# Kernel tuning notes

Measured on AMD Instinct MI355X. Metric: run time of the kernel, lower is better.

The kernel has to match this reference:

```python
import jax, jax.numpy as jnp
import numpy as np

N_NODES = 100000
N_EDGES = 3200000
IN_DIM, HID, OUT_DIM = 1, 64, 1


def graph_conv(x, src, dst, ew, W_rel, b_rel, W_root):
    # PyG GraphConv (aggr='add'): out_i = W_rel @ sum_{j->i} w_ij x_j + b_rel + W_root @ x_i
    msg = x[src] * ew[:, None]                               # [E, F]
    agg = jax.ops.segment_sum(msg, dst, num_segments=N_NODES)  # [N, F]
    return agg @ W_rel + b_rel + x @ W_root


def setup_inputs() -> dict:
    key = jax.random.key(0)
    ks = jax.random.split(key, 12)
    def glorot(k, shape):
        fan_in, fan_out = shape
        lim = float(np.sqrt(6.0 / (fan_in + fan_out)))
        return jax.random.uniform(k, shape, jnp.float32, -lim, lim)
    x = jax.random.normal(ks[0], (N_NODES, IN_DIM), jnp.float32)
    edge_index = jax.random.randint(ks[1], (2, N_EDGES), 0, N_NODES, jnp.int64)
    edge_weight = jax.random.uniform(ks[2], (N_EDGES,), jnp.float32)
    return {
        "x": x, "edge_index": edge_index, "edge_weight": edge_weight,
        "W1_rel": glorot(ks[3], (IN_DIM, HID)), "b1": jnp.zeros((HID,), jnp.float32),
        "W1_root": glorot(ks[4], (IN_DIM, HID)),
        "W2_rel": glorot(ks[5], (HID, HID)), "b2": jnp.zeros((HID,), jnp.float32),
        "W2_root": glorot(ks[6], (HID, HID)),
        "W3_rel": glorot(ks[7], (HID, OUT_DIM)), "b3": jnp.zeros((OUT_DIM,), jnp.float32),
        "W3_root": glorot(ks[8], (HID, OUT_DIM)),
    }


def reference(x, edge_index, edge_weight, W1_rel, b1, W1_root, W2_rel, b2, W2_root, W3_rel, b3, W3_root):
    src, dst = edge_index[0], edge_index[1]
    h = graph_conv(x, src, dst, edge_weight, W1_rel, b1, W1_root)
    h = jax.nn.relu(h)  # dropout is identity in eval mode
    h = graph_conv(h, src, dst, edge_weight, W2_rel, b2, W2_root)
    h = jax.nn.relu(h)
    return graph_conv(h, src, dst, edge_weight, W3_rel, b3, W3_root)
```

## Files before the change

kernel.cpp:

```cpp
#include <hip/hip_runtime.h>

#define NN 100000
#define NE 3200000
#define HID 64
#define NPB 256
#define NB  ((NN + NPB - 1) / NPB)
#define NNP (NB * NPB)
#define CAP 9216
#define MNP 128
#define NMW (2 * NB)
#define CAPW 5120
#define CHUNK 4096
#define NCH ((NE + CHUNK - 1) / CHUNK)
#define AP 72
#define BPITCH 136
#define SRCM 0x1FFFF

typedef _Float16 half8 __attribute__((ext_vector_type(8)));
typedef _Float16 h2v   __attribute__((ext_vector_type(2)));
typedef float f32x4 __attribute__((ext_vector_type(4)));

__device__ __forceinline__ unsigned short f2hb(float v) {
    _Float16 h = (_Float16)v;
    unsigned short s;
    __builtin_memcpy(&s, &h, 2);
    return s;
}
__device__ __forceinline__ h2v ash2(unsigned int u) {
    h2v r;
    __builtin_memcpy(&r, &u, 4);
    return r;
}

__global__ __launch_bounds__(512) void k_init(int* __restrict__ gcur) {
    if (threadIdx.x < NB) gcur[threadIdx.x] = threadIdx.x * CAP;
}

__global__ __launch_bounds__(256) void k_scatter(const int* __restrict__ src,
                                                 const int* __restrict__ dst,
                                                 const float* __restrict__ ew,
                                                 int* __restrict__ gcur,
                                                 int2* __restrict__ rec,
                                                 unsigned char* __restrict__ dlb) {
    __shared__ int2 lrec[CHUNK];
    __shared__ unsigned short lb[CHUNK];
    __shared__ unsigned short sidx[CHUNK];
    __shared__ int cnt[NB];
    __shared__ int bme[NB];
    __shared__ int wt8[8];
    const int tid = threadIdx.x;
    const int lane = tid & 63, wvx = tid >> 6;
    for (int j = tid; j < NB; j += 256) cnt[j] = 0;
    __syncthreads();
    const long long b0 = (long long)blockIdx.x * CHUNK;
    const int valid = (int)min((long long)CHUNK, (long long)NE - b0);
    #pragma unroll
    for (int k = 0; k < CHUNK / 256; ++k) {
        int idx = k * 256 + tid;
        if (idx < valid) {
            long long e = b0 + idx;
            int d = dst[e];
            int b = d >> 8;
            lrec[idx] = make_int2(src[e] | ((d & 255) << 17), __float_as_int(ew[e]));
            lb[idx] = (unsigned short)b;
            atomicAdd(&cnt[b], 1);
        }
    }
    __syncthreads();
    int v0 = (tid < NB) ? cnt[tid] : 0;
    int v1 = (tid + 256 < NB) ? cnt[tid + 256] : 0;
    int i0 = v0, i1 = v1;
    #pragma unroll
    for (int off = 1; off < 64; off <<= 1) {
        int t0 = __shfl_up(i0, off, 64);
        int t1 = __shfl_up(i1, off, 64);
        if (lane >= off) { i0 += t0; i1 += t1; }
    }
    if (lane == 63) { wt8[wvx] = i0; wt8[4 + wvx] = i1; }
    __syncthreads();
    int off0 = 0, off1 = 0;
    #pragma unroll
    for (int j = 0; j < 8; ++j) {
        int wt = wt8[j];
        if (j < wvx) off0 += wt;
        if (j < 4 + wvx) off1 += wt;
    }
    const int excl0 = off0 + i0 - v0;
    const int excl1 = off1 + i1 - v1;
    if (tid < NB) {
        int bb = v0 ? atomicAdd(&gcur[tid], v0) : 0;
        bme[tid] = bb - excl0;
        cnt[tid] = excl0;
    }
    if (tid + 256 < NB) {
        int bb = v1 ? atomicAdd(&gcur[tid + 256], v1) : 0;
        bme[tid + 256] = bb - excl1;
        cnt[tid + 256] = excl1;
    }
    __syncthreads();
    #pragma unroll
    for (int k = 0; k < CHUNK / 256; ++k) {
        int idx = k * 256 + tid;
        if (idx < valid) {
            int sp = atomicAdd(&cnt[lb[idx]], 1);
            sidx[sp] = (unsigned short)idx;
        }
    }
    __syncthreads();
    #pragma unroll
    for (int k = 0; k < CHUNK / 256; ++k) {
        int sp = k * 256 + tid;
        if (sp < valid) {
            int idx = sidx[sp];
            int b = lb[idx];
            int2 rc = lrec[idx];
            int go = bme[b] + sp;
            rec[go] = rc;
            dlb[go] = (unsigned char)((rc.x >> 17) & 255);
        }
    }
}

__global__ __launch_bounds__(512) void k_s1(const int* __restrict__ gcur,
                                            const int2* __restrict__ rec,
                                            const float* __restrict__ x,
                                            float2* __restrict__ sx) {
    __shared__ float loc[NPB];
    if (threadIdx.x < NPB) loc[threadIdx.x] = 0.f;
    __syncthreads();
    const int b = blockIdx.x;
    const int beg = b * CAP, cnt = gcur[b] - beg;
    for (int t = threadIdx.x; t < cnt; t += 512) {
        int2 rc = rec[beg + t];
        atomicAdd(&loc[rc.x >> 17], __int_as_float(rc.y) * x[rc.x & SRCM]);
    }
    __syncthreads();
    int i = b * NPB + threadIdx.x;
    if (threadIdx.x < NPB && i < NN) sx[i] = make_float2(loc[threadIdx.x], x[i]);
}

__global__ __launch_bounds__(512) void k_pack(const int* __restrict__ gcur,
                                              const int2* __restrict__ rec,
                                              const unsigned char* __restrict__ dlb,
                                              const float2* __restrict__ sx,
                                              int4* __restrict__ rec2q,
                                              int* __restrict__ noff,
                                              unsigned char* __restrict__ ngrp) {
    __shared__ int4 img4[CAPW / 2];
    __shared__ int hist[128];
    __shared__ int exclp[128];
    __shared__ int cur[128];
    __shared__ int wt2[2];
    unsigned short* imgh = (unsigned short*)img4;
    const int tid = threadIdx.x;
    const int lane = tid & 63, wv = tid >> 6;
    const int wid = blockIdx.x;
    const int b = wid >> 1, h = wid & 1;
    for (int j = tid; j < CAPW / 2; j += 512) img4[j] = (int4){0, 0, 0, 0};
    if (tid < 128) hist[tid] = 0;
    __syncthreads();
    const int beg = b * CAP;
    const int cnt = gcur[b] - beg;
    {
        const uchar4* d4 = (const uchar4*)(dlb + beg);
        const int n4 = cnt >> 2;
        for (int t = tid; t < n4; t += 512) {
            uchar4 q = d4[t];
            if ((q.x >> 7) == h) atomicAdd(&hist[q.x & 127], 1);
            if ((q.y >> 7) == h) atomicAdd(&hist[q.y & 127], 1);
            if ((q.z >> 7) == h) atomicAdd(&hist[q.z & 127], 1);
            if ((q.w >> 7) == h) atomicAdd(&hist[q.w & 127], 1);
        }
        for (int t = (n4 << 2) + tid; t < cnt; t += 512) {
            int dl = dlb[beg + t];
            if ((dl >> 7) == h) atomicAdd(&hist[dl & 127], 1);
        }
    }
    __syncthreads();
    int pc = 0, incl = 0;
    if (tid < 128) { pc = (hist[tid] + 7) & ~7; incl = pc; }
    #pragma unroll
    for (int off = 1; off < 64; off <<= 1) {
        int tt = __shfl_up(incl, off, 64);
        if (lane >= off) incl += tt;
    }
    if (tid < 128 && lane == 63) wt2[wv] = incl;
    __syncthreads();
    if (tid < 128) {
        int e0 = ((tid >= 64) ? wt2[0] : 0) + incl - pc;
        exclp[tid] = e0;
        cur[tid] = e0;
        const int node = wid * MNP + tid;
        noff[node] = wid * CAPW + e0;
        ngrp[node] = (unsigned char)(pc >> 3);
    }
    __syncthreads();
#define PREC(RX, RY) {                                                  \
        const int dl_ = ((RX) >> 17) & 255;                             \
        if ((dl_ >> 7) == h) {                                          \
            const float w_ = __int_as_float(RY);                        \
            const float2 v_ = sx[(RX) & SRCM];                          \
            int gs_ = atomicAdd(&cur[dl_ & 127], 1);                    \
            int hb_ = (gs_ >> 1) * 8 + (gs_ & 1);                       \
            imgh[hb_]     = f2hb(w_ * v_.x);                            \
            imgh[hb_ + 2] = f2hb(w_ * v_.y);                            \
            imgh[hb_ + 4] = f2hb(w_);                                   \
        } }
    {
        const int4* r4 = (const int4*)(rec + beg);
        const int n2 = cnt >> 1;
        for (int t = tid; t < n2; t += 512) {
            int4 q = r4[t];
            PREC(q.x, q.y)
            PREC(q.z, q.w)
        }
        for (int t = (n2 << 1) + tid; t < cnt; t += 512) {
            int2 rc = rec[beg + t];
            PREC(rc.x, rc.y)
        }
    }
#undef PREC
    __syncthreads();
    int4* d4 = rec2q + (size_t)wid * (CAPW / 2);
    for (int j = tid; j < CAPW / 2; j += 512) d4[j] = img4[j];
}

__global__ __launch_bounds__(512) void k_mega(
        const int* __restrict__ noff, const unsigned char* __restrict__ ngrp,
        const char* __restrict__ rec2b, const float2* __restrict__ sx,
        const float* __restrict__ W1_rel, const float* __restrict__ W1_root,
        const float* __restrict__ b1,
        const float* __restrict__ W2_rel, const float* __restrict__ b2,
        const float* __restrict__ W2_root,
        const float* __restrict__ W3_rel, const float* __restrict__ W3_root,
        float* __restrict__ p, float* __restrict__ r) {
    __shared__ _Float16 aggh[MNP * AP];
    __shared__ _Float16 Bt[HID * BPITCH];
    __shared__ float2 sxl[MNP];
    const int tid = threadIdx.x;
    const int f = tid & 63;
    const int wv = tid >> 6;
    const int gi0 = blockIdx.x * MNP;

    for (int j = tid; j < MNP * AP / 2; j += 512) ((int*)aggh)[j] = 0;
    for (int idx = tid; idx < HID * HID; idx += 512) {
        int k = idx >> 6, n = idx & 63;
        Bt[n * BPITCH + k]       = (_Float16)W2_rel[idx];
        Bt[n * BPITCH + HID + k] = (_Float16)W2_root[idx];
    }
    if (tid < MNP) {
        int gi = gi0 + tid;
        sxl[tid] = (gi < NN) ? sx[gi] : make_float2(0.f, 0.f);
    }
    const float w1rf = W1_rel[f], w1tf = W1_root[f], b1ff = b1[f];
    __syncthreads();

    {
        const int first = gi0 + wv * 16;
        int soff = __builtin_amdgcn_readfirstlane(noff[first]);
        const int4 gvv = *(const int4*)(ngrp + first);
        unsigned ua = __builtin_amdgcn_readfirstlane((unsigned)gvv.x);
        unsigned ub = __builtin_amdgcn_readfirstlane((unsigned)gvv.y);
        unsigned uc = __builtin_amdgcn_readfirstlane((unsigned)gvv.z);
        unsigned ud = __builtin_amdgcn_readfirstlane((unsigned)gvv.w);
        unsigned long long clo = (unsigned long long)ua | ((unsigned long long)ub << 32);
        unsigned long long chi = (unsigned long long)uc | ((unsigned long long)ud << 32);
        #define BSUM(u) (((u) & 255u) + (((u) >> 8) & 255u) + (((u) >> 16) & 255u) + ((u) >> 24))
        const int tg = (int)(BSUM(ua) + BSUM(ub) + BSUM(uc) + BSUM(ud));
        #undef BSUM

        const h2v w1r2 = {(_Float16)w1rf, (_Float16)w1rf};
        const h2v w1t2 = {(_Float16)w1tf, (_Float16)w1tf};
        const h2v b1f2 = {(_Float16)b1ff, (_Float16)b1ff};
        const h2v one2 = {(_Float16)1.f, (_Float16)1.f};
        const h2v zero2 = {(_Float16)0.f, (_Float16)0.f};

        float a0 = 0.f, a1 = 0.f, a2 = 0.f, a3 = 0.f;
        int nrow = wv * 16;
        const int rowend = nrow + 16;
        int grem = (int)(clo & 255); clo = (clo >> 8) | (chi << 56); chi >>= 8;
        while (grem == 0 && nrow + 1 < rowend) {
            ++nrow; grem = (int)(clo & 255);
            clo = (clo >> 8) | (chi << 56); chi >>= 8;
        }

        const int4* rp = (const int4*)rec2b + (soff >> 1);
        int4 A0, A1, A2, A3, B0, B1, B2, B3, C0, C1, C2, C3, D0, D1, D2, D3;
        if (tg >= 1) { A0 = rp[0]; A1 = rp[1]; A2 = rp[2];  A3 = rp[3]; }
        if (tg >= 2) { B0 = rp[4]; B1 = rp[5]; B2 = rp[6];  B3 = rp[7]; }
        if (tg >= 3) { C0 = rp[8]; C1 = rp[9]; C2 = rp[10]; C3 = rp[11]; }
        rp += 12;

#define PP(Q, AA) {                                          \
        h2v z_ = ash2((unsigned)(Q).z) * b1f2;               \
        z_ = ash2((unsigned)(Q).y) * w1t2 + z_;              \
        z_ = ash2((unsigned)(Q).x) * w1r2 + z_;              \
        z_ = __builtin_elementwise_max(z_, zero2);           \
        AA = __builtin_amdgcn_fdot2(z_, one2, AA, false); }

#define BNDRY() {                                                        \
        if (--grem == 0) {                                               \
            aggh[nrow * AP + f] = (_Float16)((a0 + a1) + (a2 + a3));     \
            a0 = a1 = a2 = a3 = 0.f;                                     \
            ++nrow; grem = (int)(clo & 255);                             \
            clo = (clo >> 8) | (chi << 56); chi >>= 8;                   \
            while (grem == 0 && nrow + 1 < rowend) {                     \
                ++nrow; grem = (int)(clo & 255);                         \
                clo = (clo >> 8) | (chi << 56); chi >>= 8;               \
            }                                                            \
        } }

        int t = 0;
        while (t + 4 <= tg) {
            D0 = rp[0]; D1 = rp[1]; D2 = rp[2]; D3 = rp[3];
            PP(A0, a0) PP(A1, a1) PP(A2, a2) PP(A3, a3) BNDRY(); ++t;
            A0 = rp[4]; A1 = rp[5]; A2 = rp[6]; A3 = rp[7];
            PP(B0, a0) PP(B1, a1) PP(B2, a2) PP(B3, a3) BNDRY(); ++t;
            B0 = rp[8]; B1 = rp[9]; B2 = rp[10]; B3 = rp[11];
            PP(C0, a0) PP(C1, a1) PP(C2, a2) PP(C3, a3) BNDRY(); ++t;
            C0 = rp[12]; C1 = rp[13]; C2 = rp[14]; C3 = rp[15];
            PP(D0, a0) PP(D1, a1) PP(D2, a2) PP(D3, a3) BNDRY(); ++t;
            rp += 16;
        }
        if (t < tg) {
            PP(A0, a0) PP(A1, a1) PP(A2, a2) PP(A3, a3) BNDRY(); ++t;
            if (t < tg) {
                PP(B0, a0) PP(B1, a1) PP(B2, a2) PP(B3, a3) BNDRY(); ++t;
                if (t < tg) {
                    PP(C0, a0) PP(C1, a1) PP(C2, a2) PP(C3, a3) BNDRY(); ++t;
                }
            }
        }
#undef PP
#undef BNDRY
    }
    __syncthreads();

    const int m16 = tid & 15;
    const int quad = (tid & 63) >> 4;
    f32x4 acc[4];
    #pragma unroll
    for (int c_ = 0; c_ < 4; ++c_) acc[c_] = (f32x4){0.f, 0.f, 0.f, 0.f};

    const float2 sm = sxl[wv * 16 + m16];

    #pragma unroll
    for (int kt = 0; kt < 4; ++kt) {
        const int kk = kt * 32;
        half8 af;
        if (kt < 2) {
            af = *(const half8*)&aggh[(wv * 16 + m16) * AP + kk + quad * 8];
        } else {
            const int fk0 = (kt - 2) * 32 + quad * 8;
            #pragma unroll
            for (int j = 0; j < 8; ++j) {
                const float wr = W1_rel[fk0 + j], wt = W1_root[fk0 + j], bb = b1[fk0 + j];
                af[j] = (_Float16)fmaxf(0.f, fmaf(sm.x, wr, fmaf(sm.y, wt, bb)));
            }
        }
        #pragma unroll
        for (int ct = 0; ct < 4; ++ct) {
            const half8 bfrag = *(const half8*)&Bt[(ct * 16 + m16) * BPITCH + kk + quad * 8];
            acc[ct] = __builtin_amdgcn_mfma_f32_16x16x32_f16(af, bfrag, acc[ct], 0, 0, 0);
        }
    }

    float b2c[4], w3rc[4], w3tc[4];
    #pragma unroll
    for (int ct = 0; ct < 4; ++ct) {
        const int col = ct * 16 + m16;
        b2c[ct] = b2[col]; w3rc[ct] = W3_rel[col]; w3tc[ct] = W3_root[col];
    }
    float pv[4] = {0.f, 0.f, 0.f, 0.f}, rv[4] = {0.f, 0.f, 0.f, 0.f};
    #pragma unroll
    for (int ct = 0; ct < 4; ++ct) {
        #pragma unroll
        for (int reg = 0; reg < 4; ++reg) {
            const float h2_ = fmaxf(0.f, acc[ct][reg] + b2c[ct]);
            pv[reg] = fmaf(h2_, w3rc[ct], pv[reg]);
            rv[reg] = fmaf(h2_, w3tc[ct], rv[reg]);
        }
    }
    #pragma unroll
    for (int reg = 0; reg < 4; ++reg) {
        #pragma unroll
        for (int msk = 1; msk < 16; msk <<= 1) {
            pv[reg] += __shfl_xor(pv[reg], msk, 64);
            rv[reg] += __shfl_xor(rv[reg], msk, 64);
        }
    }
    if (m16 == 0) {
        #pragma unroll
        for (int reg = 0; reg < 4; ++reg) {
            const int gi = gi0 + wv * 16 + quad * 4 + reg;
            if (gi < NN) { p[gi] = pv[reg]; r[gi] = rv[reg]; }
        }
    }
}

__global__ __launch_bounds__(512) void k_out(const int* __restrict__ gcur,
                                             const int2* __restrict__ rec,
                                             const float* __restrict__ pp,
                                             const float* __restrict__ rr,
                                             const float* __restrict__ b3,
                                             float* __restrict__ out) {
    __shared__ float loc[NPB];
    if (threadIdx.x < NPB) loc[threadIdx.x] = 0.f;
    __syncthreads();
    const int b = blockIdx.x;
    const int beg = b * CAP, cnt = gcur[b] - beg;
    for (int t = threadIdx.x; t < cnt; t += 512) {
        int2 rc = rec[beg + t];
        atomicAdd(&loc[rc.x >> 17], __int_as_float(rc.y) * pp[rc.x & SRCM]);
    }
    __syncthreads();
    int i = b * NPB + threadIdx.x;
    if (threadIdx.x < NPB && i < NN) out[i] = loc[threadIdx.x] + rr[i] + b3[0];
}

extern "C" void kernel_launch(void* const* d_in, const int* in_sizes, int n_in,
                              void* d_out, int out_size, void* d_ws, size_t ws_size,
                              hipStream_t stream) {
    const float* x       = (const float*)d_in[0];
    const int*   ei      = (const int*)  d_in[1];
    const float* ew      = (const float*)d_in[2];
    const float* W1_rel  = (const float*)d_in[3];
    const float* b1      = (const float*)d_in[4];
    const float* W1_root = (const float*)d_in[5];
    const float* W2_rel  = (const float*)d_in[6];
    const float* b2      = (const float*)d_in[7];
    const float* W2_root = (const float*)d_in[8];
    const float* W3_rel  = (const float*)d_in[9];
    const float* b3      = (const float*)d_in[10];
    const float* W3_root = (const float*)d_in[11];

    const int* src = ei;
    const int* dst = ei + NE;

    const size_t REC_SLOTS = (size_t)NB * CAP;
    int2*          rec   = (int2*)d_ws;
    float2*        sx    = (float2*)(rec + REC_SLOTS);
    float*         p     = (float*)(sx + NN);
    float*         r     = p + NN;
    int*           noff  = (int*)(r + NN);
    unsigned char* ngrp  = (unsigned char*)(noff + NNP);
    int*           gcur  = (int*)(ngrp + NNP);
    unsigned char* dlb   = (unsigned char*)(gcur + NB);
    char*          tail  = (char*)(dlb + REC_SLOTS);
    size_t         off   = ((size_t)(tail - (char*)d_ws) + 15) & ~(size_t)15;
    char*          rec2  = (char*)d_ws + off;

    k_init<<<1, 512, 0, stream>>>(gcur);
    k_scatter<<<NCH, 256, 0, stream>>>(src, dst, ew, gcur, rec, dlb);
    k_s1<<<NB, 512, 0, stream>>>(gcur, rec, x, sx);
    k_pack<<<NMW, 512, 0, stream>>>(gcur, rec, dlb, sx, (int4*)rec2, noff, ngrp);
    k_mega<<<NMW, 512, 0, stream>>>(noff, ngrp, rec2, sx,
                                    W1_rel, W1_root, b1,
                                    W2_rel, b2, W2_root,
                                    W3_rel, W3_root, p, r);
    k_out<<<NB, 512, 0, stream>>>(gcur, rec, p, r, b3, (float*)d_out);
}
```

Measured before the change: 259.6 us.

## Split per-bucket edge aggregation across two blocks and halve scatter chunk

k_s1 and k_out now launch two blocks per 256-node bucket, each processing half of the bucket's edges and merging its partial sums into global memory with atomicAdd. k_init pre-initializes sx with the root features, and k_mega writes the root term plus bias straight into the output, so the r buffer goes away. The scatter chunk size is halved to give more scatter blocks. This aims to raise parallelism, since only about 391 blocks ran before, at the cost of global atomics, an extra init pass, and nondeterministic float summation order.

```diff
diff --git a/kernel.cpp b/kernel.cpp
--- a/kernel.cpp
+++ b/kernel.cpp
@@ -10,7 +10,7 @@
 #define MNP 128
 #define NMW (2 * NB)
 #define CAPW 5120
-#define CHUNK 4096
+#define CHUNK 2048
 #define NCH ((NE + CHUNK - 1) / CHUNK)
 #define AP 72
 #define BPITCH 136
@@ -32,8 +32,12 @@
     return r;
 }
 
-__global__ __launch_bounds__(512) void k_init(int* __restrict__ gcur) {
-    if (threadIdx.x < NB) gcur[threadIdx.x] = threadIdx.x * CAP;
+__global__ __launch_bounds__(512) void k_init(const float* __restrict__ x,
+                                              float2* __restrict__ sx,
+                                              int* __restrict__ gcur) {
+    const int i = blockIdx.x * 512 + threadIdx.x;
+    if (i < NN) sx[i] = make_float2(0.f, x[i]);
+    if (blockIdx.x == 0 && threadIdx.x < NB) gcur[threadIdx.x] = threadIdx.x * CAP;
 }
 
 __global__ __launch_bounds__(256) void k_scatter(const int* __restrict__ src,
@@ -124,19 +128,26 @@
 __global__ __launch_bounds__(512) void k_s1(const int* __restrict__ gcur,
                                             const int2* __restrict__ rec,
                                             const float* __restrict__ x,
-                                            float2* __restrict__ sx) {
+                                            float* __restrict__ sxf) {
     __shared__ float loc[NPB];
     if (threadIdx.x < NPB) loc[threadIdx.x] = 0.f;
     __syncthreads();
-    const int b = blockIdx.x;
+    const int wid = blockIdx.x;
+    const int b = wid >> 1, j = wid & 1;
     const int beg = b * CAP, cnt = gcur[b] - beg;
-    for (int t = threadIdx.x; t < cnt; t += 512) {
-        int2 rc = rec[beg + t];
+    const int half = (cnt + 1) >> 1;
+    const int s0 = beg + j * half;
+    const int s1e = beg + min(cnt, j * half + half);
+    for (int t = s0 + threadIdx.x; t < s1e; t += 512) {
+        int2 rc = rec[t];
         atomicAdd(&loc[rc.x >> 17], __int_as_float(rc.y) * x[rc.x & SRCM]);
     }
     __syncthreads();
-    int i = b * NPB + threadIdx.x;
-    if (threadIdx.x < NPB && i < NN) sx[i] = make_float2(loc[threadIdx.x], x[i]);
+    const int i = b * NPB + threadIdx.x;
+    if (threadIdx.x < NPB && i < NN) {
+        float v = loc[threadIdx.x];
+        if (v != 0.f) atomicAdd(&sxf[2 * i], v);
+    }
 }
 
 __global__ __launch_bounds__(512) void k_pack(const int* __restrict__ gcur,
@@ -233,7 +244,8 @@
         const float* __restrict__ W2_rel, const float* __restrict__ b2,
         const float* __restrict__ W2_root,
         const float* __restrict__ W3_rel, const float* __restrict__ W3_root,
-        float* __restrict__ p, float* __restrict__ r) {
+        const float* __restrict__ b3,
+        float* __restrict__ p, float* __restrict__ out) {
     __shared__ _Float16 aggh[MNP * AP];
     __shared__ _Float16 Bt[HID * BPITCH];
     __shared__ float2 sxl[MNP];
@@ -253,6 +265,7 @@
         sxl[tid] = (gi < NN) ? sx[gi] : make_float2(0.f, 0.f);
     }
     const float w1rf = W1_rel[f], w1tf = W1_root[f], b1ff = b1[f];
+    const float b3v = b3[0];
     __syncthreads();
 
     {
@@ -393,7 +406,7 @@
         #pragma unroll
         for (int reg = 0; reg < 4; ++reg) {
             const int gi = gi0 + wv * 16 + quad * 4 + reg;
-            if (gi < NN) { p[gi] = pv[reg]; r[gi] = rv[reg]; }
+            if (gi < NN) { p[gi] = pv[reg]; out[gi] = rv[reg] + b3v; }
         }
     }
 }
@@ -401,21 +414,26 @@
 __global__ __launch_bounds__(512) void k_out(const int* __restrict__ gcur,
                                              const int2* __restrict__ rec,
                                              const float* __restrict__ pp,
-                                             const float* __restrict__ rr,
-                                             const float* __restrict__ b3,
                                              float* __restrict__ out) {
     __shared__ float loc[NPB];
     if (threadIdx.x < NPB) loc[threadIdx.x] = 0.f;
     __syncthreads();
-    const int b = blockIdx.x;
+    const int wid = blockIdx.x;
+    const int b = wid >> 1, j = wid & 1;
     const int beg = b * CAP, cnt = gcur[b] - beg;
-    for (int t = threadIdx.x; t < cnt; t += 512) {
-        int2 rc = rec[beg + t];
+    const int half = (cnt + 1) >> 1;
+    const int s0 = beg + j * half;
+    const int s1e = beg + min(cnt, j * half + half);
+    for (int t = s0 + threadIdx.x; t < s1e; t += 512) {
+        int2 rc = rec[t];
         atomicAdd(&loc[rc.x >> 17], __int_as_float(rc.y) * pp[rc.x & SRCM]);
     }
     __syncthreads();
-    int i = b * NPB + threadIdx.x;
-    if (threadIdx.x < NPB && i < NN) out[i] = loc[threadIdx.x] + rr[i] + b3[0];
+    const int i = b * NPB + threadIdx.x;
+    if (threadIdx.x < NPB && i < NN) {
+        float v = loc[threadIdx.x];
+        if (v != 0.f) atomicAdd(&out[i], v);
+    }
 }
 
 extern "C" void kernel_launch(void* const* d_in, const int* in_sizes, int n_in,
@@ -441,8 +459,7 @@
     int2*          rec   = (int2*)d_ws;
     float2*        sx    = (float2*)(rec + REC_SLOTS);
     float*         p     = (float*)(sx + NN);
-    float*         r     = p + NN;
-    int*           noff  = (int*)(r + NN);
+    int*           noff  = (int*)(p + NN);
     unsigned char* ngrp  = (unsigned char*)(noff + NNP);
     int*           gcur  = (int*)(ngrp + NNP);
     unsigned char* dlb   = (unsigned char*)(gcur + NB);
@@ -450,13 +467,13 @@
     size_t         off   = ((size_t)(tail - (char*)d_ws) + 15) & ~(size_t)15;
     char*          rec2  = (char*)d_ws + off;
 
-    k_init<<<1, 512, 0, stream>>>(gcur);
+    k_init<<<(NN + 511) / 512, 512, 0, stream>>>(x, sx, gcur);
     k_scatter<<<NCH, 256, 0, stream>>>(src, dst, ew, gcur, rec, dlb);
-    k_s1<<<NB, 512, 0, stream>>>(gcur, rec, x, sx);
+    k_s1<<<2 * NB, 512, 0, stream>>>(gcur, rec, x, (float*)sx);
     k_pack<<<NMW, 512, 0, stream>>>(gcur, rec, dlb, sx, (int4*)rec2, noff, ngrp);
     k_mega<<<NMW, 512, 0, stream>>>(noff, ngrp, rec2, sx,
                                     W1_rel, W1_root, b1,
                                     W2_rel, b2, W2_root,
-                                    W3_rel, W3_root, p, r);
-    k_out<<<NB, 512, 0, stream>>>(gcur, rec, p, r, b3, (float*)d_out);
-}
+                                    W3_rel, W3_root, b3, p, (float*)d_out);
+    k_out<<<2 * NB, 512, 0, stream>>>(gcur, rec, p, (float*)d_out);
+}
```

Measured after the change: 269.4 us. +3.8%, slower.
